# Optimization experiments

Hardware: AMD Instinct MI355X
Metric: run time of the kernel (lower is better)

The kernel has to match this reference:

```python
import jax, jax.numpy as jnp
import numpy as np

BATCH = 262144
INPUT_DIM = 256
TREE_DEPTH = 10
NUM_LEAVES = 2 ** TREE_DEPTH


def _leaf_codes(depth):
    # codes[i, d] = d-th most-significant bit of i, matching format(i, f'0{depth}b')
    idx = np.arange(2 ** depth)[:, None]
    shifts = depth - 1 - np.arange(depth)[None, :]
    return jnp.asarray(((idx >> shifts) & 1).astype(np.float32))  # [L, D]


def setup_inputs() -> dict:
    key = jax.random.key(0)
    k1, k2, k3, k4 = jax.random.split(key, 4)
    x = jax.random.normal(k1, (BATCH, INPUT_DIM), dtype=jnp.float32)
    W = jax.random.normal(k2, (INPUT_DIM, TREE_DEPTH), dtype=jnp.float32) * (1.0 / np.sqrt(INPUT_DIM))
    b = jax.random.normal(k3, (TREE_DEPTH,), dtype=jnp.float32) * 0.01
    leaf_values = jax.random.normal(k4, (NUM_LEAVES,), dtype=jnp.float32)
    return {"x": x, "W": W, "b": b, "leaf_values": leaf_values}


def reference(x, W, b, leaf_values):
    depth = W.shape[1]
    codes = _leaf_codes(depth)                      # [L, D]
    decisions = jax.nn.sigmoid(x @ W + b)           # [B, D]
    # prod over depth of (d*c + (1-d)*(1-c)) without a [B, L, D] intermediate:
    # loop over the tiny depth axis (D=10), keeping only [B, L].
    leaf_probs = jnp.ones((x.shape[0], codes.shape[0]), dtype=x.dtype)
    for d in range(depth):
        dd = decisions[:, d][:, None]               # [B, 1]
        cc = codes[:, d][None, :]                   # [1, L]
        leaf_probs = leaf_probs * (dd * cc + (1.0 - dd) * (1.0 - cc))
    out = (leaf_probs * leaf_values).sum(axis=1, keepdims=True)  # [B, 1]
    return out
```

## Files before the change

### kernel.cpp

```cpp
#include <hip/hip_runtime.h>
#include <hip/hip_bf16.h>

#define TD 10
#define NCOL 256
#define ROWS_PER_BLOCK 256
#define CHUNK_COLS 16
#define NCHUNK (NCOL / CHUNK_COLS)

typedef const __attribute__((address_space(1))) void* as1_cvp;
typedef __attribute__((address_space(3))) void* as3_vp;

__device__ __forceinline__ void gload_lds16(const float* g, float* l) {
  __builtin_amdgcn_global_load_lds((as1_cvp)(const void*)g, (as3_vp)(void*)l, 16, 0, 0);
}

template <int LEVEL, int IDX>
__device__ __forceinline__ void fold(const float* __restrict__ lv,
                                     const float (&p)[TD], const float (&q)[TD],
                                     const float (&g)[8],
                                     float prefix, float& acc) {
  if constexpr (LEVEL == TD - 3) {
    const float* l8 = lv + 8 * IDX;
    float t = l8[0] * g[0];
    t = fmaf(l8[1], g[1], t);
    t = fmaf(l8[2], g[2], t);
    t = fmaf(l8[3], g[3], t);
    t = fmaf(l8[4], g[4], t);
    t = fmaf(l8[5], g[5], t);
    t = fmaf(l8[6], g[6], t);
    t = fmaf(l8[7], g[7], t);
    acc = fmaf(prefix, t, acc);
  } else {
    fold<LEVEL + 1, 2 * IDX>(lv, p, q, g, prefix * q[LEVEL], acc);
    fold<LEVEL + 1, 2 * IDX + 1>(lv, p, q, g, prefix * p[LEVEL], acc);
  }
}

__global__ void __launch_bounds__(256, 4)
odt_kernel(const float* __restrict__ x, const float* __restrict__ W,
           const float* __restrict__ bias, const float* __restrict__ lv,
           float* __restrict__ out) {
  __shared__ float xs[4][2][64 * CHUNK_COLS];

  const int lane = threadIdx.x & 63;
  const int wave = threadIdx.x >> 6;
  const int row0 = blockIdx.x * ROWS_PER_BLOCK + wave * 64;
  const float* __restrict__ xw = x + (size_t)row0 * NCOL;

  auto stage = [&](int chunk, int buf) {
    const float* src0 = xw + chunk * CHUNK_COLS;
#pragma unroll
    for (int i = 0; i < 4; ++i) {
      const int r = i * 16 + (lane >> 2);
      const int c = ((lane & 3) ^ (r & 3)) << 2;
      gload_lds16(src0 + (size_t)r * NCOL + c, &xs[wave][buf][i * 256]);
    }
  };

  float sums[TD];
#pragma unroll
  for (int d = 0; d < TD; ++d) sums[d] = bias[d];

  stage(0, 0);

  for (int chunk = 0; chunk < NCHUNK; ++chunk) {
    const int buf = chunk & 1;
    if (chunk < NCHUNK - 1) {
      stage(chunk + 1, buf ^ 1);
      asm volatile("s_waitcnt vmcnt(4)" ::: "memory");
    } else {
      asm volatile("s_waitcnt vmcnt(0)" ::: "memory");
    }
#pragma unroll
    for (int c4 = 0; c4 < CHUNK_COLS / 4; ++c4) {
      const float4 xv = *(const float4*)&xs[wave][buf][lane * CHUNK_COLS +
                                                       ((c4 ^ (lane & 3)) << 2)];
#pragma unroll
      for (int e = 0; e < 4; ++e) {
        const float xe = (&xv.x)[e];
        const int col = chunk * CHUNK_COLS + c4 * 4 + e;
#pragma unroll
        for (int d = 0; d < TD; ++d)
          sums[d] = fmaf(xe, W[col * TD + d], sums[d]);
      }
    }
  }

  float p[TD], q[TD];
#pragma unroll
  for (int d = 0; d < TD; ++d) {
    const float s = 1.0f / (1.0f + __expf(-sums[d]));
    p[d] = s;
    q[d] = 1.0f - s;
  }

  float g[8];
  {
    const float h00 = q[8] * q[9], h01 = q[8] * p[9];
    const float h10 = p[8] * q[9], h11 = p[8] * p[9];
    g[0] = q[7] * h00; g[1] = q[7] * h01; g[2] = q[7] * h10; g[3] = q[7] * h11;
    g[4] = p[7] * h00; g[5] = p[7] * h01; g[6] = p[7] * h10; g[7] = p[7] * h11;
  }

  float acc = 0.0f;
  fold<0, 0>(lv, p, q, g, 1.0f, acc);

  out[row0 + lane] = acc;
}

extern "C" void kernel_launch(void* const* d_in, const int* in_sizes, int n_in,
                              void* d_out, int out_size, void* d_ws, size_t ws_size,
                              hipStream_t stream) {
  const float* x = (const float*)d_in[0];
  const float* W = (const float*)d_in[1];
  const float* b = (const float*)d_in[2];
  const float* lv = (const float*)d_in[3];
  float* out = (float*)d_out;

  const int batch = in_sizes[0] / NCOL;
  const int grid = batch / ROWS_PER_BLOCK;
  odt_kernel<<<grid, 256, 0, stream>>>(x, W, b, lv, out);
}
```

Before: 66.53 us.

## Stage x through registers with single LDS buffer and wider chunks

Drops the direct global-to-LDS async loads and double buffering. Each chunk is now loaded into registers with float4 global loads, overlapped with compute on the current LDS tile, then written into a single LDS buffer per wave. Chunk width doubles to 32 columns with an 8-way XOR swizzle. This halves LDS use and the number of loop iterations, at the cost of 8 extra float4 registers per thread and LDS write/read ordering that relies on each wave reading only its own data.

Result: slower. 133.3 us (+100.4%).

```diff
diff --git a/kernel.cpp b/kernel.cpp
--- a/kernel.cpp
+++ b/kernel.cpp
@@ -4,15 +4,8 @@
 #define TD 10
 #define NCOL 256
 #define ROWS_PER_BLOCK 256
-#define CHUNK_COLS 16
+#define CHUNK_COLS 32
 #define NCHUNK (NCOL / CHUNK_COLS)
-
-typedef const __attribute__((address_space(1))) void* as1_cvp;
-typedef __attribute__((address_space(3))) void* as3_vp;
-
-__device__ __forceinline__ void gload_lds16(const float* g, float* l) {
-  __builtin_amdgcn_global_load_lds((as1_cvp)(const void*)g, (as3_vp)(void*)l, 16, 0, 0);
-}
 
 template <int LEVEL, int IDX>
 __device__ __forceinline__ void fold(const float* __restrict__ lv,
@@ -40,49 +33,56 @@
 odt_kernel(const float* __restrict__ x, const float* __restrict__ W,
            const float* __restrict__ bias, const float* __restrict__ lv,
            float* __restrict__ out) {
-  __shared__ float xs[4][2][64 * CHUNK_COLS];
+  __shared__ float xs[4][64 * CHUNK_COLS];
 
   const int lane = threadIdx.x & 63;
   const int wave = threadIdx.x >> 6;
   const int row0 = blockIdx.x * ROWS_PER_BLOCK + wave * 64;
   const float* __restrict__ xw = x + (size_t)row0 * NCOL;
 
-  auto stage = [&](int chunk, int buf) {
-    const float* src0 = xw + chunk * CHUNK_COLS;
+  const int rsub = lane >> 3;
+  const int gran = lane & 7;
+  const int swz  = (gran ^ rsub) << 2;
+  const size_t gsrc = (size_t)(lane >> 3) * NCOL + gran * 4;
+  float* __restrict__ xsw = xs[wave];
+
+  float4 rbuf[8];
+
 #pragma unroll
-    for (int i = 0; i < 4; ++i) {
-      const int r = i * 16 + (lane >> 2);
-      const int c = ((lane & 3) ^ (r & 3)) << 2;
-      gload_lds16(src0 + (size_t)r * NCOL + c, &xs[wave][buf][i * 256]);
-    }
-  };
+  for (int j = 0; j < 8; ++j)
+    rbuf[j] = *(const float4*)(xw + (size_t)j * 8 * NCOL + gsrc);
+#pragma unroll
+  for (int j = 0; j < 8; ++j)
+    *(float4*)&xsw[(j * 8 + rsub) * CHUNK_COLS + swz] = rbuf[j];
 
   float sums[TD];
 #pragma unroll
   for (int d = 0; d < TD; ++d) sums[d] = bias[d];
 
-  stage(0, 0);
-
   for (int chunk = 0; chunk < NCHUNK; ++chunk) {
-    const int buf = chunk & 1;
     if (chunk < NCHUNK - 1) {
-      stage(chunk + 1, buf ^ 1);
-      asm volatile("s_waitcnt vmcnt(4)" ::: "memory");
-    } else {
-      asm volatile("s_waitcnt vmcnt(0)" ::: "memory");
+#pragma unroll
+      for (int j = 0; j < 8; ++j)
+        rbuf[j] = *(const float4*)(xw + (size_t)j * 8 * NCOL +
+                                   (chunk + 1) * CHUNK_COLS + gsrc);
     }
 #pragma unroll
-    for (int c4 = 0; c4 < CHUNK_COLS / 4; ++c4) {
-      const float4 xv = *(const float4*)&xs[wave][buf][lane * CHUNK_COLS +
-                                                       ((c4 ^ (lane & 3)) << 2)];
+    for (int i = 0; i < CHUNK_COLS / 4; ++i) {
+      const float4 xv = *(const float4*)&xsw[lane * CHUNK_COLS +
+                                             ((i ^ (lane & 7)) << 2)];
 #pragma unroll
       for (int e = 0; e < 4; ++e) {
         const float xe = (&xv.x)[e];
-        const int col = chunk * CHUNK_COLS + c4 * 4 + e;
+        const int col = chunk * CHUNK_COLS + i * 4 + e;
 #pragma unroll
         for (int d = 0; d < TD; ++d)
           sums[d] = fmaf(xe, W[col * TD + d], sums[d]);
       }
+    }
+    if (chunk < NCHUNK - 1) {
+#pragma unroll
+      for (int j = 0; j < 8; ++j)
+        *(float4*)&xsw[(j * 8 + rsub) * CHUNK_COLS + swz] = rbuf[j];
     }
   }
 
```

## Triple-buffer x staging and widen leaf-fold base case to 16 leaves

Applied to the files above, without the earlier changes.

Moves from double to triple buffering of LDS x tiles, keeping two chunks of loads in flight (vmcnt(8)) and fully unrolling the chunk loop. The tree fold now bottoms out at 16-leaf groups using a precomputed 16-entry product of the last four levels, which cuts the number of prefix multiplies. Occupancy hint drops from 4 to 3 blocks per CU, trading latency hiding through occupancy for deeper prefetch and more registers.

Result: slower. 84.70 us (+27.3%).

```diff
diff --git a/kernel.cpp b/kernel.cpp
--- a/kernel.cpp
+++ b/kernel.cpp
@@ -6,6 +6,7 @@
 #define ROWS_PER_BLOCK 256
 #define CHUNK_COLS 16
 #define NCHUNK (NCOL / CHUNK_COLS)
+#define NBUF 3
 
 typedef const __attribute__((address_space(1))) void* as1_cvp;
 typedef __attribute__((address_space(3))) void* as3_vp;
@@ -17,18 +18,13 @@
 template <int LEVEL, int IDX>
 __device__ __forceinline__ void fold(const float* __restrict__ lv,
                                      const float (&p)[TD], const float (&q)[TD],
-                                     const float (&g)[8],
+                                     const float (&g)[16],
                                      float prefix, float& acc) {
-  if constexpr (LEVEL == TD - 3) {
-    const float* l8 = lv + 8 * IDX;
-    float t = l8[0] * g[0];
-    t = fmaf(l8[1], g[1], t);
-    t = fmaf(l8[2], g[2], t);
-    t = fmaf(l8[3], g[3], t);
-    t = fmaf(l8[4], g[4], t);
-    t = fmaf(l8[5], g[5], t);
-    t = fmaf(l8[6], g[6], t);
-    t = fmaf(l8[7], g[7], t);
+  if constexpr (LEVEL == TD - 4) {
+    const float* l16 = lv + 16 * IDX;
+    float t = l16[0] * g[0];
+#pragma unroll
+    for (int k = 1; k < 16; ++k) t = fmaf(l16[k], g[k], t);
     acc = fmaf(prefix, t, acc);
   } else {
     fold<LEVEL + 1, 2 * IDX>(lv, p, q, g, prefix * q[LEVEL], acc);
@@ -36,11 +32,11 @@
   }
 }
 
-__global__ void __launch_bounds__(256, 4)
+__global__ void __launch_bounds__(256, 3)
 odt_kernel(const float* __restrict__ x, const float* __restrict__ W,
            const float* __restrict__ bias, const float* __restrict__ lv,
            float* __restrict__ out) {
-  __shared__ float xs[4][2][64 * CHUNK_COLS];
+  __shared__ float xs[4][NBUF][64 * CHUNK_COLS];
 
   const int lane = threadIdx.x & 63;
   const int wave = threadIdx.x >> 6;
@@ -62,19 +58,23 @@
   for (int d = 0; d < TD; ++d) sums[d] = bias[d];
 
   stage(0, 0);
+  stage(1, 1);
 
+#pragma unroll
   for (int chunk = 0; chunk < NCHUNK; ++chunk) {
-    const int buf = chunk & 1;
-    if (chunk < NCHUNK - 1) {
-      stage(chunk + 1, buf ^ 1);
+    if (chunk < NCHUNK - 2) {
+      stage(chunk + 2, (chunk + 2) % NBUF);
+      asm volatile("s_waitcnt vmcnt(8)" ::: "memory");
+    } else if (chunk == NCHUNK - 2) {
       asm volatile("s_waitcnt vmcnt(4)" ::: "memory");
     } else {
       asm volatile("s_waitcnt vmcnt(0)" ::: "memory");
     }
+    const float* __restrict__ xb = xs[wave][chunk % NBUF];
 #pragma unroll
     for (int c4 = 0; c4 < CHUNK_COLS / 4; ++c4) {
-      const float4 xv = *(const float4*)&xs[wave][buf][lane * CHUNK_COLS +
-                                                       ((c4 ^ (lane & 3)) << 2)];
+      const float4 xv = *(const float4*)&xb[lane * CHUNK_COLS +
+                                            ((c4 ^ (lane & 3)) << 2)];
 #pragma unroll
       for (int e = 0; e < 4; ++e) {
         const float xe = (&xv.x)[e];
@@ -94,12 +94,13 @@
     q[d] = 1.0f - s;
   }
 
-  float g[8];
+  float g[16];
   {
-    const float h00 = q[8] * q[9], h01 = q[8] * p[9];
-    const float h10 = p[8] * q[9], h11 = p[8] * p[9];
-    g[0] = q[7] * h00; g[1] = q[7] * h01; g[2] = q[7] * h10; g[3] = q[7] * h11;
-    g[4] = p[7] * h00; g[5] = p[7] * h01; g[6] = p[7] * h10; g[7] = p[7] * h11;
+    float hA[4], hB[4];
+    hA[0] = q[6] * q[7]; hA[1] = q[6] * p[7]; hA[2] = p[6] * q[7]; hA[3] = p[6] * p[7];
+    hB[0] = q[8] * q[9]; hB[1] = q[8] * p[9]; hB[2] = p[8] * q[9]; hB[3] = p[8] * p[9];
+#pragma unroll
+    for (int o = 0; o < 16; ++o) g[o] = hA[o >> 2] * hB[o & 3];
   }
 
   float acc = 0.0f;
```
